# Performance work log

Hardware: AMD Instinct MI355X
Metric: run time of the kernel (lower is better)

Reference implementation:

```python
import jax, jax.numpy as jnp
import numpy as np

SAT_LO, SAT_HI = -1.0, 1.0  # args_dict['saturations']


def setup_inputs() -> dict:
    key = jax.random.key(0)
    ks = jax.random.split(key, 6)
    B, T, n = 256, 512, 1024
    std = 1.0 / np.sqrt(n)
    x = jax.random.normal(ks[0], (B, T), jnp.float32)
    state0 = jnp.zeros((n,), jnp.float32)
    mask = jnp.ones((n,), jnp.float32)
    # 2x2 recurrent mixing matrix, scaled roughly to spectral radius ~init_radius
    w = 0.9 * jax.random.normal(ks[1], (2, 2), jnp.float32) * std * np.sqrt(n)
    dec_orth = jax.random.normal(ks[2], (n,), jnp.float32) * std
    enc_orth = jax.random.normal(ks[3], (n,), jnp.float32) * std
    decoder = jax.random.normal(ks[4], (n,), jnp.float32) * std
    encoder = jax.random.normal(ks[5], (n,), jnp.float32) * std
    return {"x": x, "state0": state0, "mask": mask, "w": w,
            "dec_orth": dec_orth, "enc_orth": enc_orth,
            "decoder": decoder, "encoder": encoder}


def reference(x, state0, mask, w, dec_orth, enc_orth, decoder, encoder):
    # W = sum_ij w[i,j] * v_i (x) v_j with v_0 = dec_orth, v_1 = enc_orth  -> [n, n]
    W = (w[0, 0] * jnp.outer(dec_orth, dec_orth)
         + w[0, 1] * jnp.outer(dec_orth, enc_orth)
         + w[1, 0] * jnp.outer(enc_orth, dec_orth)
         + w[1, 1] * jnp.outer(enc_orth, enc_orth))
    B = x.shape[0]
    n = state0.shape[0]
    s0 = jnp.zeros((B, n), x.dtype) + state0  # broadcast init state to batch

    def step(s, xt):
        # external current: encoder * x_t  -> [B, n]
        pre = (s + mask * (encoder * xt[:, None])) @ W.T
        s_new = mask * jnp.clip(pre, SAT_LO, SAT_HI)
        out = s_new @ decoder  # [B]
        return s_new, out

    _, outs = jax.lax.scan(step, s0, x.T)  # outs: [T, B]
    return outs.T  # [B, T]
```

## Files before the change

kernel.cpp:

```cpp
#include <hip/hip_runtime.h>


typedef float f32x2 __attribute__((ext_vector_type(2)));

constexpr int Bc = 256;
constexpr int Tc = 512;
constexpr int CH = Tc / 64;

__device__ __forceinline__ float readlane_f(float v, int l) {
    return __int_as_float(__builtin_amdgcn_readlane(__float_as_int(v), l));
}

#define WAVE_REDUCE3_READ(h1, h2, h3, s1, s2, s3)                                                  \
    asm("s_nop 1\n\t"                                                                              \
        "v_add_f32_dpp %[a], %[a], %[a] row_shr:1 row_mask:0xf bank_mask:0xf bound_ctrl:1\n\t"     \
        "v_add_f32_dpp %[b], %[b], %[b] row_shr:1 row_mask:0xf bank_mask:0xf bound_ctrl:1\n\t"     \
        "v_add_f32_dpp %[c], %[c], %[c] row_shr:1 row_mask:0xf bank_mask:0xf bound_ctrl:1\n\t"     \
        "v_add_f32_dpp %[a], %[a], %[a] row_shr:2 row_mask:0xf bank_mask:0xf bound_ctrl:1\n\t"     \
        "v_add_f32_dpp %[b], %[b], %[b] row_shr:2 row_mask:0xf bank_mask:0xf bound_ctrl:1\n\t"     \
        "v_add_f32_dpp %[c], %[c], %[c] row_shr:2 row_mask:0xf bank_mask:0xf bound_ctrl:1\n\t"     \
        "v_add_f32_dpp %[a], %[a], %[a] row_shr:4 row_mask:0xf bank_mask:0xf bound_ctrl:1\n\t"     \
        "v_add_f32_dpp %[b], %[b], %[b] row_shr:4 row_mask:0xf bank_mask:0xf bound_ctrl:1\n\t"     \
        "v_add_f32_dpp %[c], %[c], %[c] row_shr:4 row_mask:0xf bank_mask:0xf bound_ctrl:1\n\t"     \
        "v_add_f32_dpp %[a], %[a], %[a] row_shr:8 row_mask:0xf bank_mask:0xf bound_ctrl:1\n\t"     \
        "v_add_f32_dpp %[b], %[b], %[b] row_shr:8 row_mask:0xf bank_mask:0xf bound_ctrl:1\n\t"     \
        "v_add_f32_dpp %[c], %[c], %[c] row_shr:8 row_mask:0xf bank_mask:0xf bound_ctrl:1\n\t"     \
        "v_add_f32_dpp %[a], %[a], %[a] row_bcast:15 row_mask:0xa bank_mask:0xf\n\t"               \
        "v_add_f32_dpp %[b], %[b], %[b] row_bcast:15 row_mask:0xa bank_mask:0xf\n\t"               \
        "v_add_f32_dpp %[c], %[c], %[c] row_bcast:15 row_mask:0xa bank_mask:0xf\n\t"               \
        "v_add_f32_dpp %[a], %[a], %[a] row_bcast:31 row_mask:0xc bank_mask:0xf\n\t"               \
        "v_add_f32_dpp %[b], %[b], %[b] row_bcast:31 row_mask:0xc bank_mask:0xf\n\t"               \
        "v_add_f32_dpp %[c], %[c], %[c] row_bcast:31 row_mask:0xc bank_mask:0xf\n\t"               \
        "v_readlane_b32 %[x], %[a], 63\n\t"                                                        \
        "v_readlane_b32 %[y], %[b], 63\n\t"                                                        \
        "v_readlane_b32 %[z], %[c], 63"                                                            \
        : [a] "+v"(h1), [b] "+v"(h2), [c] "+v"(h3),                                                \
          [x] "=s"(s1), [y] "=s"(s2), [z] "=s"(s3))

#define DECL_TBL(i) f32x2 d2_##i, e2_##i, g1_##i, g2_##i, wo_##i

#define INIT_TBL(i) do { \
    _Pragma("unroll") \
    for (int h = 0; h < 2; ++h) { \
        const int c = lane + 64 * (2 * (i) + h); \
        const float dv   = dec_orth[c]; \
        const float ev   = enc_orth[c]; \
        const float mv   = mask[c]; \
        const float encv = encoder[c]; \
        const float decv = decoder[c]; \
        const float s0v  = state0[c]; \
        const float mdv = mv * dv, mev = mv * ev; \
        d2_##i[h]  = dv;  e2_##i[h]  = ev; \
        g1_##i[h] = fmaf(w00, mdv, w01 * mev); \
        g2_##i[h] = fmaf(w10, mdv, w11 * mev); \
        wo_##i[h] = mv * decv; \
        s0d += s0v * dv;  s0e += s0v * ev; \
        kd = fmaf(mv * encv, dv, kd); \
        ke = fmaf(mv * encv, ev, ke); \
    } \
} while (0)

#define ACC_J(i, A1V, A2V, AOV) do { \
    f32x2 tt = r2 * e2_##i + d2_##i;                  \
    f32x2 mm; \
    mm.x = __builtin_amdgcn_fmed3f(tt.x, nb, bb); \
    mm.y = __builtin_amdgcn_fmed3f(tt.y, nb, bb); \
    A1V += mm * g1_##i; \
    A2V += mm * g2_##i; \
    AOV += mm * wo_##i; \
} while (0)

__global__ __attribute__((amdgpu_waves_per_eu(1, 1))) __launch_bounds__(64)
void twotwonet_kernel(
    const float* __restrict__ x,
    const float* __restrict__ state0,
    const float* __restrict__ mask,
    const float* __restrict__ w,
    const float* __restrict__ dec_orth,
    const float* __restrict__ enc_orth,
    const float* __restrict__ decoder,
    const float* __restrict__ encoder,
    float* __restrict__ out)
{
    const int b    = blockIdx.x;
    const int lane = threadIdx.x;

    const float w00 = w[0], w01 = w[1], w10 = w[2], w11 = w[3];

    DECL_TBL(0); DECL_TBL(1); DECL_TBL(2); DECL_TBL(3);
    DECL_TBL(4); DECL_TBL(5); DECL_TBL(6); DECL_TBL(7);

    float s0d = 0.f, s0e = 0.f, kd = 0.f, ke = 0.f;
    INIT_TBL(0); INIT_TBL(1); INIT_TBL(2); INIT_TBL(3);
    INIT_TBL(4); INIT_TBL(5); INIT_TBL(6); INIT_TBL(7);

#pragma unroll
    for (int m = 32; m >= 1; m >>= 1) {
        s0d += __shfl_xor(s0d, m, 64);
        s0e += __shfl_xor(s0e, m, 64);
        kd  += __shfl_xor(kd, m, 64);
        ke  += __shfl_xor(ke, m, 64);
    }

    const float A1 = fmaf(w00, kd, w01 * ke);
    const float A2 = fmaf(w10, kd, w11 * ke);

    const float* xrow = x + (size_t)b * Tc;
    float xr[CH];
#pragma unroll
    for (int c = 0; c < CH; ++c) xr[c] = xrow[lane + 64 * c];

    float au = 1.0f;
    float q1 = fmaf(w00, s0d, w01 * s0e);
    float q2 = fmaf(w10, s0d, w11 * s0e);

#pragma unroll
    for (int c = 0; c < CH; ++c) {
        float obuf = 0.f;
#pragma unroll 2
        for (int t2 = 0; t2 < 64; ++t2) {
            const float xs = readlane_f(xr[c], t2);

            const float alpha = fmaf(au, q1, xs * A1);
            const float beta  = fmaf(au, q2, xs * A2);

            const float aun = copysignf(fmaxf(fabsf(alpha), 1e-20f), alpha);
            const float inv = __builtin_amdgcn_rcpf(aun);
            const float r   = beta * inv;
            const float bb  = fabsf(inv);
            const float nb  = -bb;
            const f32x2 r2  = {r, r};

            f32x2 a1a = {0.f, 0.f}, a1b = {0.f, 0.f};
            f32x2 a2a = {0.f, 0.f}, a2b = {0.f, 0.f};
            f32x2 aoa = {0.f, 0.f}, aob = {0.f, 0.f};
            ACC_J(0, a1a, a2a, aoa); ACC_J(1, a1b, a2b, aob);
            ACC_J(2, a1a, a2a, aoa); ACC_J(3, a1b, a2b, aob);
            ACC_J(4, a1a, a2a, aoa); ACC_J(5, a1b, a2b, aob);
            ACC_J(6, a1a, a2a, aoa); ACC_J(7, a1b, a2b, aob);

            const f32x2 s1v = a1a + a1b;
            const f32x2 s2v = a2a + a2b;
            const f32x2 sov = aoa + aob;
            float h1 = s1v.x + s1v.y;
            float h2 = s2v.x + s2v.y;
            float ho = sov.x + sov.y;

            float q1n, q2n, son;
            WAVE_REDUCE3_READ(h1, h2, ho, q1n, q2n, son);
            q1 = q1n;
            q2 = q2n;
            au = aun;

            const float ov = aun * son;
            obuf = (t2 == lane) ? ov : obuf;
        }
        out[(size_t)b * Tc + 64 * c + lane] = obuf;
    }
}

extern "C" void kernel_launch(void* const* d_in, const int* in_sizes, int n_in,
                              void* d_out, int out_size, void* d_ws, size_t ws_size,
                              hipStream_t stream) {
    const float* x        = (const float*)d_in[0];
    const float* state0   = (const float*)d_in[1];
    const float* mask     = (const float*)d_in[2];
    const float* w        = (const float*)d_in[3];
    const float* dec_orth = (const float*)d_in[4];
    const float* enc_orth = (const float*)d_in[5];
    const float* decoder  = (const float*)d_in[6];
    const float* encoder  = (const float*)d_in[7];
    float* out = (float*)d_out;

    twotwonet_kernel<<<dim3(Bc), dim3(64), 0, stream>>>(
        x, state0, mask, w, dec_orth, enc_orth, decoder, encoder, out);
}
```

Before: 99.39 us.

## Process two batch rows per wave and drop the rescaled-state reciprocal trick

Each wave now runs the recurrence for two batch rows at once, interleaving their independent dependency chains, and fuses the six cross-lane reductions into one DPP sequence. The launch grid is halved to 128 blocks. The per-step scale normalisation (the clamped reciprocal of alpha and the copysign guard) is replaced by direct clamping of alpha*d + beta*e to [-1,1]. This shortens the serial critical path and hides reduction latency through instruction-level parallelism. The cost is twice the per-step arithmetic per wave and only half as many waves across the 256 compute units.

```diff
diff --git a/kernel.cpp b/kernel.cpp
--- a/kernel.cpp
+++ b/kernel.cpp
@@ -11,31 +11,32 @@
     return __int_as_float(__builtin_amdgcn_readlane(__float_as_int(v), l));
 }
 
-#define WAVE_REDUCE3_READ(h1, h2, h3, s1, s2, s3)                                                  \
-    asm("s_nop 1\n\t"                                                                              \
-        "v_add_f32_dpp %[a], %[a], %[a] row_shr:1 row_mask:0xf bank_mask:0xf bound_ctrl:1\n\t"     \
-        "v_add_f32_dpp %[b], %[b], %[b] row_shr:1 row_mask:0xf bank_mask:0xf bound_ctrl:1\n\t"     \
-        "v_add_f32_dpp %[c], %[c], %[c] row_shr:1 row_mask:0xf bank_mask:0xf bound_ctrl:1\n\t"     \
-        "v_add_f32_dpp %[a], %[a], %[a] row_shr:2 row_mask:0xf bank_mask:0xf bound_ctrl:1\n\t"     \
-        "v_add_f32_dpp %[b], %[b], %[b] row_shr:2 row_mask:0xf bank_mask:0xf bound_ctrl:1\n\t"     \
-        "v_add_f32_dpp %[c], %[c], %[c] row_shr:2 row_mask:0xf bank_mask:0xf bound_ctrl:1\n\t"     \
-        "v_add_f32_dpp %[a], %[a], %[a] row_shr:4 row_mask:0xf bank_mask:0xf bound_ctrl:1\n\t"     \
-        "v_add_f32_dpp %[b], %[b], %[b] row_shr:4 row_mask:0xf bank_mask:0xf bound_ctrl:1\n\t"     \
-        "v_add_f32_dpp %[c], %[c], %[c] row_shr:4 row_mask:0xf bank_mask:0xf bound_ctrl:1\n\t"     \
-        "v_add_f32_dpp %[a], %[a], %[a] row_shr:8 row_mask:0xf bank_mask:0xf bound_ctrl:1\n\t"     \
-        "v_add_f32_dpp %[b], %[b], %[b] row_shr:8 row_mask:0xf bank_mask:0xf bound_ctrl:1\n\t"     \
-        "v_add_f32_dpp %[c], %[c], %[c] row_shr:8 row_mask:0xf bank_mask:0xf bound_ctrl:1\n\t"     \
-        "v_add_f32_dpp %[a], %[a], %[a] row_bcast:15 row_mask:0xa bank_mask:0xf\n\t"               \
-        "v_add_f32_dpp %[b], %[b], %[b] row_bcast:15 row_mask:0xa bank_mask:0xf\n\t"               \
-        "v_add_f32_dpp %[c], %[c], %[c] row_bcast:15 row_mask:0xa bank_mask:0xf\n\t"               \
-        "v_add_f32_dpp %[a], %[a], %[a] row_bcast:31 row_mask:0xc bank_mask:0xf\n\t"               \
-        "v_add_f32_dpp %[b], %[b], %[b] row_bcast:31 row_mask:0xc bank_mask:0xf\n\t"               \
-        "v_add_f32_dpp %[c], %[c], %[c] row_bcast:31 row_mask:0xc bank_mask:0xf\n\t"               \
-        "v_readlane_b32 %[x], %[a], 63\n\t"                                                        \
-        "v_readlane_b32 %[y], %[b], 63\n\t"                                                        \
-        "v_readlane_b32 %[z], %[c], 63"                                                            \
-        : [a] "+v"(h1), [b] "+v"(h2), [c] "+v"(h3),                                                \
-          [x] "=s"(s1), [y] "=s"(s2), [z] "=s"(s3))
+#define DPP6(lvl, msk)                                                                              \
+        "v_add_f32_dpp %[a], %[a], %[a] " lvl " row_mask:" msk " bank_mask:0xf bound_ctrl:1\n\t"    \
+        "v_add_f32_dpp %[b], %[b], %[b] " lvl " row_mask:" msk " bank_mask:0xf bound_ctrl:1\n\t"    \
+        "v_add_f32_dpp %[c], %[c], %[c] " lvl " row_mask:" msk " bank_mask:0xf bound_ctrl:1\n\t"    \
+        "v_add_f32_dpp %[d], %[d], %[d] " lvl " row_mask:" msk " bank_mask:0xf bound_ctrl:1\n\t"    \
+        "v_add_f32_dpp %[e], %[e], %[e] " lvl " row_mask:" msk " bank_mask:0xf bound_ctrl:1\n\t"    \
+        "v_add_f32_dpp %[f], %[f], %[f] " lvl " row_mask:" msk " bank_mask:0xf bound_ctrl:1\n\t"
+
+#define WAVE_REDUCE6_READ(h1, h2, h3, h4, h5, h6, s1, s2, s3, s4, s5, s6)                           \
+    asm("s_nop 1\n\t"                                                                               \
+        DPP6("row_shr:1",   "0xf")                                                                  \
+        DPP6("row_shr:2",   "0xf")                                                                  \
+        DPP6("row_shr:4",   "0xf")                                                                  \
+        DPP6("row_shr:8",   "0xf")                                                                  \
+        DPP6("row_bcast:15","0xa")                                                                  \
+        DPP6("row_bcast:31","0xc")                                                                  \
+        "v_readlane_b32 %[x], %[a], 63\n\t"                                                         \
+        "v_readlane_b32 %[y], %[b], 63\n\t"                                                         \
+        "v_readlane_b32 %[z], %[c], 63\n\t"                                                         \
+        "v_readlane_b32 %[u], %[d], 63\n\t"                                                         \
+        "v_readlane_b32 %[v], %[e], 63\n\t"                                                         \
+        "v_readlane_b32 %[w], %[f], 63"                                                             \
+        : [a] "+v"(h1), [b] "+v"(h2), [c] "+v"(h3),                                                 \
+          [d] "+v"(h4), [e] "+v"(h5), [f] "+v"(h6),                                                 \
+          [x] "=s"(s1), [y] "=s"(s2), [z] "=s"(s3),                                                 \
+          [u] "=s"(s4), [v] "=s"(s5), [w] "=s"(s6))
 
 #define DECL_TBL(i) f32x2 d2_##i, e2_##i, g1_##i, g2_##i, wo_##i
 
@@ -60,11 +61,11 @@
     } \
 } while (0)
 
-#define ACC_J(i, A1V, A2V, AOV) do { \
-    f32x2 tt = r2 * e2_##i + d2_##i;                  \
+#define ACC_J(i, al, be, A1V, A2V, AOV) do { \
+    f32x2 tt = (al) * d2_##i + (be) * e2_##i; \
     f32x2 mm; \
-    mm.x = __builtin_amdgcn_fmed3f(tt.x, nb, bb); \
-    mm.y = __builtin_amdgcn_fmed3f(tt.y, nb, bb); \
+    mm.x = __builtin_amdgcn_fmed3f(tt.x, -1.0f, 1.0f); \
+    mm.y = __builtin_amdgcn_fmed3f(tt.y, -1.0f, 1.0f); \
     A1V += mm * g1_##i; \
     A2V += mm * g2_##i; \
     AOV += mm * wo_##i; \
@@ -82,7 +83,7 @@
     const float* __restrict__ encoder,
     float* __restrict__ out)
 {
-    const int b    = blockIdx.x;
+    const int b0   = 2 * blockIdx.x;
     const int lane = threadIdx.x;
 
     const float w00 = w[0], w01 = w[1], w10 = w[2], w11 = w[3];
@@ -105,57 +106,57 @@
     const float A1 = fmaf(w00, kd, w01 * ke);
     const float A2 = fmaf(w10, kd, w11 * ke);
 
-    const float* xrow = x + (size_t)b * Tc;
-    float xr[CH];
+    const float* xrowA = x + (size_t)b0 * Tc;
+    const float* xrowB = x + (size_t)(b0 + 1) * Tc;
+    float xrA[CH], xrB[CH];
 #pragma unroll
-    for (int c = 0; c < CH; ++c) xr[c] = xrow[lane + 64 * c];
+    for (int c = 0; c < CH; ++c) { xrA[c] = xrowA[lane + 64 * c]; xrB[c] = xrowB[lane + 64 * c]; }
 
-    float au = 1.0f;
-    float q1 = fmaf(w00, s0d, w01 * s0e);
-    float q2 = fmaf(w10, s0d, w11 * s0e);
+    float q1A = fmaf(w00, s0d, w01 * s0e);
+    float q2A = fmaf(w10, s0d, w11 * s0e);
+    float q1B = q1A, q2B = q2A;
 
 #pragma unroll
     for (int c = 0; c < CH; ++c) {
-        float obuf = 0.f;
+        float obufA = 0.f, obufB = 0.f;
 #pragma unroll 2
         for (int t2 = 0; t2 < 64; ++t2) {
-            const float xs = readlane_f(xr[c], t2);
+            const float xsA = readlane_f(xrA[c], t2);
+            const float xsB = readlane_f(xrB[c], t2);
 
-            const float alpha = fmaf(au, q1, xs * A1);
-            const float beta  = fmaf(au, q2, xs * A2);
+            const float alA = fmaf(xsA, A1, q1A);
+            const float beA = fmaf(xsA, A2, q2A);
+            const float alB = fmaf(xsB, A1, q1B);
+            const float beB = fmaf(xsB, A2, q2B);
+            const f32x2 a2A = {alA, alA}, b2A = {beA, beA};
+            const f32x2 a2B = {alB, alB}, b2B = {beB, beB};
 
-            const float aun = copysignf(fmaxf(fabsf(alpha), 1e-20f), alpha);
-            const float inv = __builtin_amdgcn_rcpf(aun);
-            const float r   = beta * inv;
-            const float bb  = fabsf(inv);
-            const float nb  = -bb;
-            const f32x2 r2  = {r, r};
+            f32x2 p1A = {0.f, 0.f}, p2A = {0.f, 0.f}, poA = {0.f, 0.f};
+            f32x2 p1B = {0.f, 0.f}, p2B = {0.f, 0.f}, poB = {0.f, 0.f};
+            ACC_J(0, a2A, b2A, p1A, p2A, poA);  ACC_J(0, a2B, b2B, p1B, p2B, poB);
+            ACC_J(1, a2A, b2A, p1A, p2A, poA);  ACC_J(1, a2B, b2B, p1B, p2B, poB);
+            ACC_J(2, a2A, b2A, p1A, p2A, poA);  ACC_J(2, a2B, b2B, p1B, p2B, poB);
+            ACC_J(3, a2A, b2A, p1A, p2A, poA);  ACC_J(3, a2B, b2B, p1B, p2B, poB);
+            ACC_J(4, a2A, b2A, p1A, p2A, poA);  ACC_J(4, a2B, b2B, p1B, p2B, poB);
+            ACC_J(5, a2A, b2A, p1A, p2A, poA);  ACC_J(5, a2B, b2B, p1B, p2B, poB);
+            ACC_J(6, a2A, b2A, p1A, p2A, poA);  ACC_J(6, a2B, b2B, p1B, p2B, poB);
+            ACC_J(7, a2A, b2A, p1A, p2A, poA);  ACC_J(7, a2B, b2B, p1B, p2B, poB);
 
-            f32x2 a1a = {0.f, 0.f}, a1b = {0.f, 0.f};
-            f32x2 a2a = {0.f, 0.f}, a2b = {0.f, 0.f};
-            f32x2 aoa = {0.f, 0.f}, aob = {0.f, 0.f};
-            ACC_J(0, a1a, a2a, aoa); ACC_J(1, a1b, a2b, aob);
-            ACC_J(2, a1a, a2a, aoa); ACC_J(3, a1b, a2b, aob);
-            ACC_J(4, a1a, a2a, aoa); ACC_J(5, a1b, a2b, aob);
-            ACC_J(6, a1a, a2a, aoa); ACC_J(7, a1b, a2b, aob);
+            float h1A = p1A.x + p1A.y, h2A = p2A.x + p2A.y, hoA = poA.x + poA.y;
+            float h1B = p1B.x + p1B.y, h2B = p2B.x + p2B.y, hoB = poB.x + poB.y;
 
-            const f32x2 s1v = a1a + a1b;
-            const f32x2 s2v = a2a + a2b;
-            const f32x2 sov = aoa + aob;
-            float h1 = s1v.x + s1v.y;
-            float h2 = s2v.x + s2v.y;
-            float ho = sov.x + sov.y;
+            float r1A, r2A, roA, r1B, r2B, roB;
+            WAVE_REDUCE6_READ(h1A, h2A, hoA, h1B, h2B, hoB,
+                              r1A, r2A, roA, r1B, r2B, roB);
+            q1A = r1A; q2A = r2A;
+            q1B = r1B; q2B = r2B;
 
-            float q1n, q2n, son;
-            WAVE_REDUCE3_READ(h1, h2, ho, q1n, q2n, son);
-            q1 = q1n;
-            q2 = q2n;
-            au = aun;
-
-            const float ov = aun * son;
-            obuf = (t2 == lane) ? ov : obuf;
+            const bool mine = (t2 == lane);
+            obufA = mine ? roA : obufA;
+            obufB = mine ? roB : obufB;
         }
-        out[(size_t)b * Tc + 64 * c + lane] = obuf;
+        out[(size_t)b0 * Tc + 64 * c + lane]       = obufA;
+        out[(size_t)(b0 + 1) * Tc + 64 * c + lane] = obufB;
     }
 }
 
@@ -172,6 +173,6 @@
     const float* encoder  = (const float*)d_in[7];
     float* out = (float*)d_out;
 
-    twotwonet_kernel<<<dim3(Bc), dim3(64), 0, stream>>>(
+    twotwonet_kernel<<<dim3(Bc / 2), dim3(64), 0, stream>>>(
         x, state0, mask, w, dec_orth, enc_orth, decoder, encoder, out);
 }
```

Measured after the change: 188.5 us. 89.7% more time.
